# Optimization experiments

Measured on AMD Instinct MI355X. Metric: run time of the kernel, lower is better.

## Reference

```python
import jax, jax.numpy as jnp
import numpy as np

T, B, I, H = 512, 32, 512, 1024


def setup_inputs() -> dict:
    key = jax.random.key(0)
    ks = jax.random.split(key, 32)
    si = 1.0 / np.sqrt(I)
    sh = 1.0 / np.sqrt(H)
    inp = {
        'X': jax.random.normal(ks[0], (T, B, I), jnp.float32),
        'h0': jax.random.normal(ks[1], (B, H), jnp.float32),
        'c0': jax.random.normal(ks[2], (B, H), jnp.float32),
        'w_ii': jax.random.normal(ks[3], (H, I), jnp.float32) * si,
        'w_hi': jax.random.normal(ks[4], (H, H), jnp.float32) * sh,
        'w_ci': jax.random.normal(ks[5], (H, H), jnp.float32) * sh,
        'w_if': jax.random.normal(ks[6], (H, I), jnp.float32) * si,
        'w_hf': jax.random.normal(ks[7], (H, H), jnp.float32) * sh,
        'w_cf': jax.random.normal(ks[8], (H, H), jnp.float32) * sh,
        'w_ic': jax.random.normal(ks[9], (H, I), jnp.float32) * si,
        'w_hc': jax.random.normal(ks[10], (H, H), jnp.float32) * sh,
        'w_io': jax.random.normal(ks[11], (H, I), jnp.float32) * si,
        'w_ho': jax.random.normal(ks[12], (H, H), jnp.float32) * sh,
        'w_cyo': jax.random.normal(ks[13], (H, H), jnp.float32) * sh,
    }
    for j, name in enumerate(['b_ii', 'b_hi', 'b_ci', 'b_if', 'b_hf', 'b_cf',
                              'b_ic', 'b_hc', 'b_io', 'b_ho', 'b_cyo']):
        inp[name] = jax.random.normal(ks[14 + j], (H,), jnp.float32) * 0.01
    return inp


def reference(X, h0, c0,
              w_ii, w_hi, w_ci, w_if, w_hf, w_cf, w_ic, w_hc, w_io, w_ho, w_cyo,
              b_ii, b_hi, b_ci, b_if, b_hf, b_cf, b_ic, b_hc, b_io, b_ho, b_cyo):
    # Precompute all input projections for the whole sequence (one big GEMM per gate),
    # folding in the constant biases. Shapes: [T, B, H].
    xi = jnp.einsum('tbi,hi->tbh', X, w_ii) + (b_ii + b_hi + b_ci)
    xf = jnp.einsum('tbi,hi->tbh', X, w_if) + (b_if + b_hf + b_cf)
    xg = jnp.einsum('tbi,hi->tbh', X, w_ic) + (b_ic + b_hc)
    xo = jnp.einsum('tbi,hi->tbh', X, w_io) + (b_io + b_ho + b_cyo)

    def step(carry, xs):
        h, c = carry  # [B, H]
        pi, pf, pg, po = xs
        i = jax.nn.sigmoid(pi + h @ w_hi.T + c @ w_ci.T)   # input gate (peephole on c_{t-1})
        f = jax.nn.sigmoid(pf + h @ w_hf.T + c @ w_cf.T)   # forget gate (peephole on c_{t-1})
        g = jnp.tanh(pg + h @ w_hc.T)                      # proposed cell state
        cy = f * c + i * g
        o = jax.nn.sigmoid(po + h @ w_ho.T + cy @ w_cyo.T)  # output gate (peephole on c_t)
        hy = o * jnp.tanh(cy)
        return (hy, cy), hy

    _, out = jax.lax.scan(step, (h0, c0), (xi, xf, xg, xo))
    return out  # [T, B, H]
```

## Files before the change

kernel.cpp:

```cpp
#include <hip/hip_runtime.h>
#include <math.h>

#define T_LEN 512
#define B_SZ  32
#define I_DIM 512
#define H_DIM 1024
#define NBLK  256
#define HS    (B_SZ * H_DIM)
#define WROW  1028

typedef float fx4 __attribute__((ext_vector_type(4)));

__global__ void bias_combine(const float* __restrict__ b_ii, const float* __restrict__ b_hi,
                             const float* __restrict__ b_ci, const float* __restrict__ b_if,
                             const float* __restrict__ b_hf, const float* __restrict__ b_cf,
                             const float* __restrict__ b_ic, const float* __restrict__ b_hc,
                             const float* __restrict__ b_io, const float* __restrict__ b_ho,
                             const float* __restrict__ b_cyo, float* __restrict__ bias4) {
    int r = blockIdx.x * 256 + threadIdx.x;
    if (r < H_DIM) {
        bias4[r]        = b_ii[r] + b_hi[r] + b_ci[r];
        bias4[1024 + r] = b_if[r] + b_hf[r] + b_cf[r];
        bias4[2048 + r] = b_ic[r] + b_hc[r];
        bias4[3072 + r] = b_io[r] + b_ho[r] + b_cyo[r];
    }
}

#define BM 128
#define BN 128
#define BK 16
__global__ __launch_bounds__(256) void pregemm(const float* __restrict__ A,
                                               const float* __restrict__ w0,
                                               const float* __restrict__ w1,
                                               const float* __restrict__ w2,
                                               const float* __restrict__ w3,
                                               const float* __restrict__ bias4,
                                               float* __restrict__ C, int M) {
    __shared__ float As[BK][BM + 4];
    __shared__ float Bs[BK][BN + 4];
    int tid = threadIdx.x;
    int n0 = blockIdx.y * BN;
    const float* W = (n0 < 1024) ? w0 : (n0 < 2048) ? w1 : (n0 < 3072) ? w2 : w3;
    int nloc = n0 & 1023;

    int lr = tid >> 2;
    int lk = (tid & 3) << 2;
    const float* Arow = A + (size_t)(blockIdx.x * BM + lr) * I_DIM + lk;
    const float* Brow = W + (size_t)(nloc + lr) * I_DIM + lk;

    float acc[8][8];
#pragma unroll
    for (int i = 0; i < 8; ++i)
#pragma unroll
        for (int j = 0; j < 8; ++j) acc[i][j] = 0.f;

    int mth = (tid >> 4) << 3;
    int nth = (tid & 15) << 3;

    for (int kt = 0; kt < I_DIM; kt += BK) {
        float4 a0 = *(const float4*)(Arow + kt);
        float4 a1 = *(const float4*)(Arow + 64 * I_DIM + kt);
        float4 b0 = *(const float4*)(Brow + kt);
        float4 b1 = *(const float4*)(Brow + 64 * I_DIM + kt);
        __syncthreads();
        As[lk + 0][lr] = a0.x; As[lk + 1][lr] = a0.y; As[lk + 2][lr] = a0.z; As[lk + 3][lr] = a0.w;
        As[lk + 0][lr + 64] = a1.x; As[lk + 1][lr + 64] = a1.y; As[lk + 2][lr + 64] = a1.z; As[lk + 3][lr + 64] = a1.w;
        Bs[lk + 0][lr] = b0.x; Bs[lk + 1][lr] = b0.y; Bs[lk + 2][lr] = b0.z; Bs[lk + 3][lr] = b0.w;
        Bs[lk + 0][lr + 64] = b1.x; Bs[lk + 1][lr + 64] = b1.y; Bs[lk + 2][lr + 64] = b1.z; Bs[lk + 3][lr + 64] = b1.w;
        __syncthreads();
#pragma unroll
        for (int j = 0; j < BK; ++j) {
            float am[8], bn[8];
            *(float4*)&am[0] = *(const float4*)&As[j][mth];
            *(float4*)&am[4] = *(const float4*)&As[j][mth + 4];
            *(float4*)&bn[0] = *(const float4*)&Bs[j][nth];
            *(float4*)&bn[4] = *(const float4*)&Bs[j][nth + 4];
#pragma unroll
            for (int ii = 0; ii < 8; ++ii)
#pragma unroll
                for (int jj = 0; jj < 8; ++jj) acc[ii][jj] += am[ii] * bn[jj];
        }
    }

    int mbase = blockIdx.x * BM + mth;
#pragma unroll
    for (int jj = 0; jj < 8; ++jj) {
        int n = n0 + nth + jj;
        float bn = bias4[n];
        float* crow = C + (size_t)n * M + mbase;
        fx4 v0, v1;
        v0.x = acc[0][jj] + bn; v0.y = acc[1][jj] + bn;
        v0.z = acc[2][jj] + bn; v0.w = acc[3][jj] + bn;
        v1.x = acc[4][jj] + bn; v1.y = acc[5][jj] + bn;
        v1.z = acc[6][jj] + bn; v1.w = acc[7][jj] + bn;
        __builtin_nontemporal_store(v0, (fx4*)crow);
        __builtin_nontemporal_store(v1, (fx4*)(crow + 4));
    }
}

__device__ __forceinline__ float sigm(float x) { return 1.f / (1.f + __expf(-x)); }
__device__ __forceinline__ float tanh_fast(float x) { return 2.f / (1.f + __expf(-2.f * x)) - 1.f; }

__device__ __forceinline__ void agent_store(float* p, float v) {
    __hip_atomic_store(p, v, __ATOMIC_RELAXED, __HIP_MEMORY_SCOPE_AGENT);
}

__device__ __forceinline__ void arrive_wait(unsigned* grp, unsigned* master,
                                            int grpid, unsigned bidx) {
    unsigned old = __hip_atomic_fetch_add(&grp[grpid * 16], 1u,
                                          __ATOMIC_RELAXED, __HIP_MEMORY_SCOPE_AGENT);
    if (old == bidx * 32u + 31u)
        __hip_atomic_fetch_add(master, 1u, __ATOMIC_RELAXED, __HIP_MEMORY_SCOPE_AGENT);
    while (__hip_atomic_load(master, __ATOMIC_RELAXED, __HIP_MEMORY_SCOPE_AGENT)
           < (bidx + 1u) * 8u)
        __builtin_amdgcn_s_sleep(1);
}

#define SMEM_FLOATS (28 * WROW + 4096 + 4096 + 512 + 512 + 128 + 128)
#define SMEM_BYTES  (SMEM_FLOATS * 4)

__global__ __launch_bounds__(512) void lstm_scan(
    const float* __restrict__ G,
    const float* __restrict__ h0,
    const float* __restrict__ c_init,
    const float* __restrict__ w_hi, const float* __restrict__ w_ci,
    const float* __restrict__ w_hf, const float* __restrict__ w_cf,
    const float* __restrict__ w_hc, const float* __restrict__ w_ho,
    const float* __restrict__ w_cyo,
    float* __restrict__ out,
    float* __restrict__ c_hist,
    unsigned* __restrict__ grp_ctr,
    unsigned* __restrict__ master,
    int t0, int Tc, int M)
{
    extern __shared__ float smem[];
    float* wAB    = smem;
    float* redA   = smem + 28 * WROW;
    float* redB   = redA + 4096;
    float* red2A  = redB + 4096;
    float* red2B  = red2A + 512;
    float* po_lds = red2B + 512;
    float* cy_lds = po_lds + 128;

    int tid = threadIdx.x;
    int blk = blockIdx.x;
    int r0 = blk * 4;
    int grpid = blk & 7;

    int wv = tid >> 6;
    int lane = tid & 63;
    int g = lane >> 3;
    int rml = lane & 7;
    int kbase = wv * 128;
    int b0 = g * 4;

    int rrm = tid >> 5;
    int rb  = tid & 31;

    {
        const float* srcs[7] = {w_hi, w_ci, w_hf, w_cf, w_hc, w_ho, w_cyo};
        for (int idx = tid; idx < 28 * 256; idx += 512) {
            int rr = idx >> 8;
            int kk = (idx & 255) << 2;
            float4 v = *(const float4*)(srcs[rr >> 2] + (size_t)(r0 + (rr & 3)) * H_DIM + kk);
            *(float4*)(wAB + rr * WROW + kk) = v;
        }
    }

    int mi1 = rml >> 2, q1 = rml & 3;
    const float* pA1 = wAB + (mi1 * 8 + q1) * WROW + kbase;
    const float* pA2 = wAB + (16 + mi1 * 4 + q1) * WROW + kbase;
    int rmA1 = mi1 * 4 + q1;
    int rmA2 = 8 + mi1 * 4 + q1;

    const float* pB1 = (rml < 4) ? (wAB + (24 + rml) * WROW + kbase)
                                 : (wAB + (4 + (rml - 4)) * WROW + kbase);
    const float* pB2 = wAB + (12 + (rml & 3)) * WROW + kbase;
    int rmB1 = rml;
    int rmB2 = 8 + rml;

    int frw = (tid >> 5) & 3;
    int fb = tid & 31;
    int fr = r0 + frw;

    __syncthreads();

    {
        const float* cb = c_init + (size_t)b0 * H_DIM + kbase;
        float s10 = 0.f, s11 = 0.f, s12 = 0.f, s13 = 0.f;
        float s20 = 0.f, s21 = 0.f, s22 = 0.f, s23 = 0.f;
#pragma unroll 8
        for (int it = 0; it < 32; ++it) {
            int k = it * 4;
            float4 c0v = *(const float4*)(cb + 0 * H_DIM + k);
            float4 c1v = *(const float4*)(cb + 1 * H_DIM + k);
            float4 c2v = *(const float4*)(cb + 2 * H_DIM + k);
            float4 c3v = *(const float4*)(cb + 3 * H_DIM + k);
            float4 wa = *(const float4*)(pB1 + k);
            float4 wb = *(const float4*)(pB2 + k);
            s10 += wa.x * c0v.x + wa.y * c0v.y + wa.z * c0v.z + wa.w * c0v.w;
            s11 += wa.x * c1v.x + wa.y * c1v.y + wa.z * c1v.z + wa.w * c1v.w;
            s12 += wa.x * c2v.x + wa.y * c2v.y + wa.z * c2v.z + wa.w * c2v.w;
            s13 += wa.x * c3v.x + wa.y * c3v.y + wa.z * c3v.z + wa.w * c3v.w;
            s20 += wb.x * c0v.x + wb.y * c0v.y + wb.z * c0v.z + wb.w * c0v.w;
            s21 += wb.x * c1v.x + wb.y * c1v.y + wb.z * c1v.z + wb.w * c1v.w;
            s22 += wb.x * c2v.x + wb.y * c2v.y + wb.z * c2v.z + wb.w * c2v.w;
            s23 += wb.x * c3v.x + wb.y * c3v.y + wb.z * c3v.z + wb.w * c3v.w;
        }
        *(float4*)(redB + (wv * 16 + rmB1) * 32 + b0) = (float4){s10, s11, s12, s13};
        *(float4*)(redB + (wv * 16 + rmB2) * 32 + b0) = (float4){s20, s21, s22, s23};
        if (tid < 128)
            cy_lds[frw * 32 + fb] = c_init[(size_t)fb * H_DIM + fr];
    }
    __syncthreads();
    {
        float v = 0.f;
#pragma unroll
        for (int w8 = 0; w8 < 8; ++w8) v += redB[(w8 * 16 + rrm) * 32 + rb];
        red2B[rrm * 32 + rb] = v;
    }
    __syncthreads();

    unsigned bidx = 0;

    for (int tt = 0; tt < Tc; ++tt) {
        int t = t0 + tt;
        const float* hp = (t == 0) ? h0 : out + (size_t)(t - 1) * HS;
        float* cw = c_hist + (size_t)(tt + 1) * HS;

        float xi = 0.f, xf = 0.f, xg = 0.f, xo = 0.f;
        if (tid < 128) {
            int m = tt * 32 + fb;
            xi = __builtin_nontemporal_load(G + (size_t)(0 * 1024 + fr) * M + m);
            xf = __builtin_nontemporal_load(G + (size_t)(1 * 1024 + fr) * M + m);
            xg = __builtin_nontemporal_load(G + (size_t)(2 * 1024 + fr) * M + m);
            xo = __builtin_nontemporal_load(G + (size_t)(3 * 1024 + fr) * M + m);
        }

        const float* hb = hp + (size_t)b0 * H_DIM + kbase;
        float a10 = 0.f, a11 = 0.f, a12 = 0.f, a13 = 0.f;
        float a20 = 0.f, a21 = 0.f, a22 = 0.f, a23 = 0.f;
#pragma unroll 8
        for (int it = 0; it < 32; ++it) {
            int k = it * 4;
            float4 h0v = *(const float4*)(hb + 0 * H_DIM + k);
            float4 h1v = *(const float4*)(hb + 1 * H_DIM + k);
            float4 h2v = *(const float4*)(hb + 2 * H_DIM + k);
            float4 h3v = *(const float4*)(hb + 3 * H_DIM + k);
            float4 wa = *(const float4*)(pA1 + k);
            float4 wb = *(const float4*)(pA2 + k);
            a10 += wa.x * h0v.x + wa.y * h0v.y + wa.z * h0v.z + wa.w * h0v.w;
            a11 += wa.x * h1v.x + wa.y * h1v.y + wa.z * h1v.z + wa.w * h1v.w;
            a12 += wa.x * h2v.x + wa.y * h2v.y + wa.z * h2v.z + wa.w * h2v.w;
            a13 += wa.x * h3v.x + wa.y * h3v.y + wa.z * h3v.z + wa.w * h3v.w;
            a20 += wb.x * h0v.x + wb.y * h0v.y + wb.z * h0v.z + wb.w * h0v.w;
            a21 += wb.x * h1v.x + wb.y * h1v.y + wb.z * h1v.z + wb.w * h1v.w;
            a22 += wb.x * h2v.x + wb.y * h2v.y + wb.z * h2v.z + wb.w * h2v.w;
            a23 += wb.x * h3v.x + wb.y * h3v.y + wb.z * h3v.z + wb.w * h3v.w;
        }
        *(float4*)(redA + (wv * 16 + rmA1) * 32 + b0) = (float4){a10, a11, a12, a13};
        *(float4*)(redA + (wv * 16 + rmA2) * 32 + b0) = (float4){a20, a21, a22, a23};
        __syncthreads();

        {
            float v = 0.f;
#pragma unroll
            for (int w8 = 0; w8 < 8; ++w8) v += redA[(w8 * 16 + rrm) * 32 + rb];
            red2A[rrm * 32 + rb] = v;
        }
        __syncthreads();

        if (tid < 128) {
            float shi = red2A[(0 + frw) * 32 + fb];
            float shf = red2A[(4 + frw) * 32 + fb];
            float shc = red2A[(8 + frw) * 32 + fb];
            float sho = red2A[(12 + frw) * 32 + fb];
            float sci = red2B[(4 + frw) * 32 + fb];
            float scf = red2B[(8 + frw) * 32 + fb];
            float iv = sigm(xi + shi + sci);
            float fv = sigm(xf + shf + scf);
            float gv = tanh_fast(xg + shc);
            float cold = cy_lds[frw * 32 + fb];
            float cy = fv * cold + iv * gv;
            agent_store(&cw[(size_t)fb * H_DIM + fr], cy);
            po_lds[frw * 32 + fb] = xo + sho;
            cy_lds[frw * 32 + fb] = cy;
        }
        __syncthreads();

        if (tid == 0) arrive_wait(grp_ctr, master, grpid, bidx);
        bidx++;
        __builtin_amdgcn_fence(__ATOMIC_ACQUIRE, "workgroup");
        __syncthreads();

        const float* cyb = cw + (size_t)b0 * H_DIM + kbase;
        float b10 = 0.f, b11 = 0.f, b12 = 0.f, b13 = 0.f;
        float b20 = 0.f, b21 = 0.f, b22 = 0.f, b23 = 0.f;
#pragma unroll 8
        for (int it = 0; it < 32; ++it) {
            int k = it * 4;
            float4 c0v = *(const float4*)(cyb + 0 * H_DIM + k);
            float4 c1v = *(const float4*)(cyb + 1 * H_DIM + k);
            float4 c2v = *(const float4*)(cyb + 2 * H_DIM + k);
            float4 c3v = *(const float4*)(cyb + 3 * H_DIM + k);
            float4 wa = *(const float4*)(pB1 + k);
            float4 wb = *(const float4*)(pB2 + k);
            b10 += wa.x * c0v.x + wa.y * c0v.y + wa.z * c0v.z + wa.w * c0v.w;
            b11 += wa.x * c1v.x + wa.y * c1v.y + wa.z * c1v.z + wa.w * c1v.w;
            b12 += wa.x * c2v.x + wa.y * c2v.y + wa.z * c2v.z + wa.w * c2v.w;
            b13 += wa.x * c3v.x + wa.y * c3v.y + wa.z * c3v.z + wa.w * c3v.w;
            b20 += wb.x * c0v.x + wb.y * c0v.y + wb.z * c0v.z + wb.w * c0v.w;
            b21 += wb.x * c1v.x + wb.y * c1v.y + wb.z * c1v.z + wb.w * c1v.w;
            b22 += wb.x * c2v.x + wb.y * c2v.y + wb.z * c2v.z + wb.w * c2v.w;
            b23 += wb.x * c3v.x + wb.y * c3v.y + wb.z * c3v.z + wb.w * c3v.w;
        }
        *(float4*)(redB + (wv * 16 + rmB1) * 32 + b0) = (float4){b10, b11, b12, b13};
        *(float4*)(redB + (wv * 16 + rmB2) * 32 + b0) = (float4){b20, b21, b22, b23};
        __syncthreads();

        {
            float v = 0.f;
#pragma unroll
            for (int w8 = 0; w8 < 8; ++w8) v += redB[(w8 * 16 + rrm) * 32 + rb];
            red2B[rrm * 32 + rb] = v;
        }
        __syncthreads();

        if (tid < 128) {
            float v = red2B[frw * 32 + fb];
            float o = sigm(po_lds[frw * 32 + fb] + v);
            float hy = o * tanh_fast(cy_lds[frw * 32 + fb]);
            agent_store(&out[(size_t)t * HS + (size_t)fb * H_DIM + fr], hy);
        }
        __syncthreads();

        if (tid == 0) arrive_wait(grp_ctr, master, grpid, bidx);
        bidx++;
        __builtin_amdgcn_fence(__ATOMIC_ACQUIRE, "workgroup");
        __syncthreads();
    }
}

extern "C" void kernel_launch(void* const* d_in, const int* in_sizes, int n_in,
                              void* d_out, int out_size, void* d_ws, size_t ws_size,
                              hipStream_t stream) {
    const float* X     = (const float*)d_in[0];
    const float* h0    = (const float*)d_in[1];
    const float* c0    = (const float*)d_in[2];
    const float* w_ii  = (const float*)d_in[3];
    const float* w_hi  = (const float*)d_in[4];
    const float* w_ci  = (const float*)d_in[5];
    const float* w_if  = (const float*)d_in[6];
    const float* w_hf  = (const float*)d_in[7];
    const float* w_cf  = (const float*)d_in[8];
    const float* w_ic  = (const float*)d_in[9];
    const float* w_hc  = (const float*)d_in[10];
    const float* w_io  = (const float*)d_in[11];
    const float* w_ho  = (const float*)d_in[12];
    const float* w_cyo = (const float*)d_in[13];
    const float* b_ii  = (const float*)d_in[14];
    const float* b_hi  = (const float*)d_in[15];
    const float* b_ci  = (const float*)d_in[16];
    const float* b_if  = (const float*)d_in[17];
    const float* b_hf  = (const float*)d_in[18];
    const float* b_cf  = (const float*)d_in[19];
    const float* b_ic  = (const float*)d_in[20];
    const float* b_hc  = (const float*)d_in[21];
    const float* b_io  = (const float*)d_in[22];
    const float* b_ho  = (const float*)d_in[23];
    const float* b_cyo = (const float*)d_in[24];
    float* out = (float*)d_out;

    (void)hipFuncSetAttribute((const void*)lstm_scan,
                              hipFuncAttributeMaxDynamicSharedMemorySize, SMEM_BYTES);

    int Tc = 512;
    while (Tc > 8) {
        size_t need = ((size_t)Tc * 131072 + 4096 + (size_t)(Tc + 1) * HS) * 4 + 2048;
        if (need <= ws_size) break;
        Tc >>= 1;
    }
    int M = Tc * 32;

    float* G      = (float*)d_ws;
    float* bias4  = G + (size_t)Tc * 131072;
    float* c_hist = bias4 + 4096;
    unsigned* grp_ctr = (unsigned*)(c_hist + (size_t)(Tc + 1) * HS);
    unsigned* master  = grp_ctr + 256;

    bias_combine<<<4, 256, 0, stream>>>(b_ii, b_hi, b_ci, b_if, b_hf, b_cf,
                                        b_ic, b_hc, b_io, b_ho, b_cyo, bias4);

    const float* c_init = c0;
    for (int t0 = 0; t0 < T_LEN; t0 += Tc) {
        pregemm<<<dim3(M / BM, 4096 / BN), 256, 0, stream>>>(
            X + (size_t)t0 * B_SZ * I_DIM, w_ii, w_if, w_ic, w_io, bias4, G, M);
        (void)hipMemsetAsync(grp_ctr, 0, 2048, stream);

        const float* Gp = G;
        float* chp = c_hist;
        unsigned* gcp = grp_ctr;
        unsigned* mp = master;
        int t0v = t0, Tcv = Tc, Mv = M;
        void* args[] = {
            (void*)&Gp, (void*)&h0, (void*)&c_init,
            (void*)&w_hi, (void*)&w_ci, (void*)&w_hf, (void*)&w_cf,
            (void*)&w_hc, (void*)&w_ho, (void*)&w_cyo,
            (void*)&out, (void*)&chp, (void*)&gcp, (void*)&mp,
            (void*)&t0v, (void*)&Tcv, (void*)&Mv
        };
        (void)hipLaunchCooperativeKernel((const void*)lstm_scan, dim3(NBLK), dim3(512),
                                         args, SMEM_BYTES, stream);
        c_init = c_hist + (size_t)Tc * HS;
    }
}
```

Baseline: 12.42 ms.

## Replace global grid barriers with per-slice dataflow counters per wavefront

Replaces the two-level all-block barrier with per-slice counters. Each block increments the counter for the 128-wide hidden slice it owns after writing cy or h. Each wavefront then waits only on the counter for the K-slice it will read. This removes the full-grid rendezvous and lets blocks start consuming data as soon as their needed slice is ready, so neighbouring phases can overlap. In exchange it adds more polling traffic, since every wavefront now polls instead of one thread per block. It also relies on the counters being zeroed per launch and on correct release/acquire ordering across chunks (t0>0).

```diff
diff --git a/kernel.cpp b/kernel.cpp
--- a/kernel.cpp
+++ b/kernel.cpp
@@ -103,17 +103,6 @@
 
 __device__ __forceinline__ void agent_store(float* p, float v) {
     __hip_atomic_store(p, v, __ATOMIC_RELAXED, __HIP_MEMORY_SCOPE_AGENT);
-}
-
-__device__ __forceinline__ void arrive_wait(unsigned* grp, unsigned* master,
-                                            int grpid, unsigned bidx) {
-    unsigned old = __hip_atomic_fetch_add(&grp[grpid * 16], 1u,
-                                          __ATOMIC_RELAXED, __HIP_MEMORY_SCOPE_AGENT);
-    if (old == bidx * 32u + 31u)
-        __hip_atomic_fetch_add(master, 1u, __ATOMIC_RELAXED, __HIP_MEMORY_SCOPE_AGENT);
-    while (__hip_atomic_load(master, __ATOMIC_RELAXED, __HIP_MEMORY_SCOPE_AGENT)
-           < (bidx + 1u) * 8u)
-        __builtin_amdgcn_s_sleep(1);
 }
 
 #define SMEM_FLOATS (28 * WROW + 4096 + 4096 + 512 + 512 + 128 + 128)
@@ -145,7 +134,7 @@
     int tid = threadIdx.x;
     int blk = blockIdx.x;
     int r0 = blk * 4;
-    int grpid = blk & 7;
+    int slice_own = blk >> 5;
 
     int wv = tid >> 6;
     int lane = tid & 63;
@@ -156,6 +145,10 @@
 
     int rrm = tid >> 5;
     int rb  = tid & 31;
+
+    unsigned* cnt_cy = grp_ctr;
+    unsigned* cnt_h  = grp_ctr + 128;
+    (void)master;
 
     {
         const float* srcs[7] = {w_hi, w_ci, w_hf, w_cf, w_hc, w_ho, w_cyo};
@@ -221,8 +214,6 @@
     }
     __syncthreads();
 
-    unsigned bidx = 0;
-
     for (int tt = 0; tt < Tc; ++tt) {
         int t = t0 + tt;
         const float* hp = (t == 0) ? h0 : out + (size_t)(t - 1) * HS;
@@ -235,6 +226,14 @@
             xf = __builtin_nontemporal_load(G + (size_t)(1 * 1024 + fr) * M + m);
             xg = __builtin_nontemporal_load(G + (size_t)(2 * 1024 + fr) * M + m);
             xo = __builtin_nontemporal_load(G + (size_t)(3 * 1024 + fr) * M + m);
+        }
+
+        if (tt > 0 || t0 > 0) {
+            unsigned tgt = 32u * (unsigned)tt;
+            while (__hip_atomic_load(&cnt_h[wv * 16], __ATOMIC_RELAXED,
+                                     __HIP_MEMORY_SCOPE_AGENT) < tgt)
+                __builtin_amdgcn_s_sleep(1);
+            __builtin_amdgcn_fence(__ATOMIC_ACQUIRE, "agent");
         }
 
         const float* hb = hp + (size_t)b0 * H_DIM + kbase;
@@ -288,10 +287,17 @@
         }
         __syncthreads();
 
-        if (tid == 0) arrive_wait(grp_ctr, master, grpid, bidx);
-        bidx++;
-        __builtin_amdgcn_fence(__ATOMIC_ACQUIRE, "workgroup");
-        __syncthreads();
+        if (tid == 0)
+            (void)__hip_atomic_fetch_add(&cnt_cy[slice_own * 16], 1u,
+                                         __ATOMIC_RELEASE, __HIP_MEMORY_SCOPE_AGENT);
+
+        {
+            unsigned tgt = 32u * (unsigned)(tt + 1);
+            while (__hip_atomic_load(&cnt_cy[wv * 16], __ATOMIC_RELAXED,
+                                     __HIP_MEMORY_SCOPE_AGENT) < tgt)
+                __builtin_amdgcn_s_sleep(1);
+            __builtin_amdgcn_fence(__ATOMIC_ACQUIRE, "agent");
+        }
 
         const float* cyb = cw + (size_t)b0 * H_DIM + kbase;
         float b10 = 0.f, b11 = 0.f, b12 = 0.f, b13 = 0.f;
@@ -334,10 +340,9 @@
         }
         __syncthreads();
 
-        if (tid == 0) arrive_wait(grp_ctr, master, grpid, bidx);
-        bidx++;
-        __builtin_amdgcn_fence(__ATOMIC_ACQUIRE, "workgroup");
-        __syncthreads();
+        if (tid == 0)
+            (void)__hip_atomic_fetch_add(&cnt_h[slice_own * 16], 1u,
+                                         __ATOMIC_RELEASE, __HIP_MEMORY_SCOPE_AGENT);
     }
 }
 
```

Result: slower. 37.11 ms (+198.7%).
